# Optimization experiments

Hardware: AMD Instinct MI355X
Metric: run time of the kernel (lower is better)

Reference implementation:

```python
import jax, jax.numpy as jnp
import numpy as np

ACT = jax.nn.leaky_relu  # Decima uses leaky_relu activations


def _mlp(x, params):
    # Linear + act chain (activation applied after every layer, incl. last, as in the torch code)
    for W, b in params:
        x = ACT(x @ W + b)
    return x


def setup_inputs() -> dict:
    key = jax.random.key(0)
    N, E, D = 500_000, 4_000_000, 8  # nodes, edges per depth, max_depth
    ks = jax.random.split(key, 32)
    inp = {}
    inp["inputs"] = jax.random.normal(ks[0], (N, 5), dtype=jnp.float32)
    inp["adj_src"] = jax.random.randint(ks[1], (D, E), 0, N, dtype=jnp.int32)
    inp["adj_dst"] = jax.random.randint(ks[2], (D, E), 0, N, dtype=jnp.int32)
    inp["masks"] = (jax.random.uniform(ks[3], (D, N, 1)) > 0.5).astype(jnp.float32)
    # MLP stacks: prep 5->16->32->8, proc/agg 8->16->32->8 (xavier-ish init, zero bias)
    dims = {"prep": [(5, 16), (16, 32), (32, 8)],
            "proc": [(8, 16), (16, 32), (32, 8)],
            "agg": [(8, 16), (16, 32), (32, 8)]}
    i = 4
    for name, ds in dims.items():
        for j, (a, b) in enumerate(ds):
            scale = np.sqrt(6.0 / (a + b)).astype(np.float32)
            inp[f"{name}_W{j}"] = jax.random.uniform(ks[i], (a, b), jnp.float32, -scale, scale)
            inp[f"{name}_b{j}"] = jnp.zeros((b,), jnp.float32)
            i += 1
    return inp


def reference(inputs, adj_src, adj_dst, masks,
              prep_W0, prep_b0, prep_W1, prep_b1, prep_W2, prep_b2,
              proc_W0, proc_b0, proc_W1, proc_b1, proc_W2, proc_b2,
              agg_W0, agg_b0, agg_W1, agg_b1, agg_W2, agg_b2):
    prep = [(prep_W0, prep_b0), (prep_W1, prep_b1), (prep_W2, prep_b2)]
    proc = [(proc_W0, proc_b0), (proc_W1, proc_b1), (proc_W2, proc_b2)]
    agg = [(agg_W0, agg_b0), (agg_W1, agg_b1), (agg_W2, agg_b2)]
    N = inputs.shape[0]
    max_depth = adj_src.shape[0]

    x = _mlp(inputs, prep)  # [N, 8]
    for d in range(max_depth):  # small fixed loop over depths
        y = _mlp(x, proc)  # [N, 8]
        # sparse adj matmul (unit-valued adjacency): out[i] = sum_{j: (i,j) in adj} y[j]
        y = jax.ops.segment_sum(y[adj_src[d]], adj_dst[d], num_segments=N)
        y = _mlp(y, agg)
        x = x + y * masks[d]  # mask + residual
    return x
```

## Files before the change

### kernel.cpp

```cpp
#include <hip/hip_runtime.h>
#include <hip/hip_fp16.h>


typedef unsigned long long u64;
typedef unsigned int u32;

#define BKT_BITS 10
#define BKT_SIZE 1024
#define MAXNB    512
#define NBLK     256

template <int CH> struct Cfg;
template <> struct Cfg<4> { static const int CAPC = 6;  static const int SUBC = 24; };
template <> struct Cfg<2> { static const int CAPC = 14; static const int SUBC = 32; };
template <> struct Cfg<1> { static const int CAPC = 30; static const int SUBC = 64; };

__device__ __forceinline__ float lrelu(float v) { return fmaxf(v, 0.01f * v); }

template <int IN>
__device__ __forceinline__ void mlp3(const float* __restrict__ xin, float* __restrict__ yout,
    const float* __restrict__ sW0, const float* __restrict__ sb0,
    const float* __restrict__ sW1, const float* __restrict__ sb1,
    const float* __restrict__ sW2, const float* __restrict__ sb2)
{
    float h1[16];
#pragma unroll
    for (int o = 0; o < 16; ++o) {
        float s = sb0[o];
#pragma unroll
        for (int a = 0; a < IN; ++a) s = fmaf(xin[a], sW0[a * 16 + o], s);
        h1[o] = lrelu(s);
    }
    float h2[32];
#pragma unroll
    for (int o = 0; o < 32; ++o) {
        float s = sb1[o];
#pragma unroll
        for (int a = 0; a < 16; ++a) s = fmaf(h1[a], sW1[a * 32 + o], s);
        h2[o] = lrelu(s);
    }
#pragma unroll
    for (int o = 0; o < 8; ++o) {
        float s = sb2[o];
#pragma unroll
        for (int a = 0; a < 32; ++a) s = fmaf(h2[a], sW2[a * 8 + o], s);
        yout[o] = lrelu(s);
    }
}

__device__ __forceinline__ void ldw(float* d, const float* s, int n) {
    for (int t = threadIdx.x; t < n; t += 256) d[t] = s[t];
}

__device__ __forceinline__ uint4 pack_h8(const float* y) {
    __half2 p0 = __floats2half2_rn(y[0], y[1]);
    __half2 p1 = __floats2half2_rn(y[2], y[3]);
    __half2 p2 = __floats2half2_rn(y[4], y[5]);
    __half2 p3 = __floats2half2_rn(y[6], y[7]);
    uint4 v;
    v.x = *(u32*)&p0; v.y = *(u32*)&p1; v.z = *(u32*)&p2; v.w = *(u32*)&p3;
    return v;
}

__global__ __launch_bounds__(256) void prep_proc_kernel(
    const float* __restrict__ in, float* __restrict__ x, uint4* __restrict__ y,
    const float* pW0, const float* pb0, const float* pW1, const float* pb1,
    const float* pW2, const float* pb2,
    const float* cW0, const float* cb0, const float* cW1, const float* cb1,
    const float* cW2, const float* cb2, int N)
{
    __shared__ float P0[80],  Pb0[16], P1[512], Pb1[32], P2[256], Pb2[8];
    __shared__ float C0[128], Cb0[16], C1[512], Cb1[32], C2[256], Cb2[8];
    ldw(P0, pW0, 80);  ldw(Pb0, pb0, 16); ldw(P1, pW1, 512); ldw(Pb1, pb1, 32);
    ldw(P2, pW2, 256); ldw(Pb2, pb2, 8);
    ldw(C0, cW0, 128); ldw(Cb0, cb0, 16); ldw(C1, cW1, 512); ldw(Cb1, cb1, 32);
    ldw(C2, cW2, 256); ldw(Cb2, cb2, 8);
    __syncthreads();
    int i = blockIdx.x * 256 + threadIdx.x;
    if (i >= N) return;
    float xin[5];
#pragma unroll
    for (int k = 0; k < 5; ++k) xin[k] = in[(size_t)i * 5 + k];
    float xv[8];
    mlp3<5>(xin, xv, P0, Pb0, P1, Pb1, P2, Pb2);
    float4* xp = (float4*)(x + 8 * (size_t)i);
    xp[0] = make_float4(xv[0], xv[1], xv[2], xv[3]);
    xp[1] = make_float4(xv[4], xv[5], xv[6], xv[7]);
    float yv[8];
    mlp3<8>(xv, yv, C0, Cb0, C1, Cb1, C2, Cb2);
    y[i] = pack_h8(yv);
}

template <bool DO_PROC, int CHUNKS>
__global__ __launch_bounds__(256) void aggproc_kernel(
    const uint4* __restrict__ acc, float* __restrict__ x, const float* __restrict__ mask,
    uint4* __restrict__ y,
    const float* aW0, const float* ab0, const float* aW1, const float* ab1,
    const float* aW2, const float* ab2,
    const float* cW0, const float* cb0, const float* cW1, const float* cb1,
    const float* cW2, const float* cb2, int N)
{
    __shared__ float A0[128], Ab0[16], A1[512], Ab1[32], A2[256], Ab2[8];
    __shared__ float C0[128], Cb0[16], C1[512], Cb1[32], C2[256], Cb2[8];
    ldw(A0, aW0, 128); ldw(Ab0, ab0, 16); ldw(A1, aW1, 512); ldw(Ab1, ab1, 32);
    ldw(A2, aW2, 256); ldw(Ab2, ab2, 8);
    if (DO_PROC) {
        ldw(C0, cW0, 128); ldw(Cb0, cb0, 16); ldw(C1, cW1, 512); ldw(Cb1, cb1, 32);
        ldw(C2, cW2, 256); ldw(Cb2, cb2, 8);
    }
    __syncthreads();
    int i = blockIdx.x * 256 + threadIdx.x;
    if (i >= N) return;
    float ain[8] = {0.f, 0.f, 0.f, 0.f, 0.f, 0.f, 0.f, 0.f};
#pragma unroll
    for (int c = 0; c < CHUNKS; ++c) {
        uint4 v = acc[(size_t)c * N + i];
        float2 f0 = __half22float2(*(__half2*)&v.x);
        float2 f1 = __half22float2(*(__half2*)&v.y);
        float2 f2 = __half22float2(*(__half2*)&v.z);
        float2 f3 = __half22float2(*(__half2*)&v.w);
        ain[0] += f0.x; ain[1] += f0.y; ain[2] += f1.x; ain[3] += f1.y;
        ain[4] += f2.x; ain[5] += f2.y; ain[6] += f3.x; ain[7] += f3.y;
    }
    float ya[8];
    mlp3<8>(ain, ya, A0, Ab0, A1, Ab1, A2, Ab2);
    float m = mask[i];
    float4* xp = (float4*)(x + 8 * (size_t)i);
    float4 x0 = xp[0], x1 = xp[1];
    float xn[8] = {x0.x + ya[0] * m, x0.y + ya[1] * m, x0.z + ya[2] * m, x0.w + ya[3] * m,
                   x1.x + ya[4] * m, x1.y + ya[5] * m, x1.z + ya[6] * m, x1.w + ya[7] * m};
    xp[0] = make_float4(xn[0], xn[1], xn[2], xn[3]);
    xp[1] = make_float4(xn[4], xn[5], xn[6], xn[7]);
    if (DO_PROC) {
        float yv[8];
        mlp3<8>(xn, yv, C0, Cb0, C1, Cb1, C2, Cb2);
        y[i] = pack_h8(yv);
    }
}

__global__ __launch_bounds__(256) void mask_pack_kernel(
    const float* __restrict__ masks, u64* __restrict__ bitmaps, int N, int D, int BITW)
{
    int i = blockIdx.x * 256 + threadIdx.x;
    int lane = threadIdx.x & 63;
    for (int d = 0; d < D; ++d) {
        bool b = (i < N) ? (masks[(size_t)d * N + i] != 0.f) : false;
        u64 m = __ballot(b);
        if (lane == 0 && i < N) bitmaps[(size_t)d * BITW + (i >> 6)] = m;
    }
}

template <int CHUNKS>
__global__ __launch_bounds__(256) void place_kernel(
    const int* __restrict__ adj_src, const int* __restrict__ adj_dst,
    const u64* __restrict__ bitmaps,
    u32* __restrict__ ebuf_all,
    int* __restrict__ cnt_all,
    int E, int NB, int shift, int BITW)
{
    constexpr int CAPC = Cfg<CHUNKS>::CAPC;
    constexpr int SUBC = Cfg<CHUNKS>::SUBC;
    const int dep = blockIdx.y;
    const int* src = adj_src + (size_t)dep * E;
    const int* dst = adj_dst + (size_t)dep * E;
    const u64* bitmap = bitmaps + (size_t)dep * BITW;
    u32* ebuf = ebuf_all + (size_t)dep * ((size_t)NB * CHUNKS * NBLK * SUBC);
    int* cnt_g = cnt_all + (size_t)dep * ((size_t)NB * CHUNKS * NBLK);

    __shared__ int lcnt[MAXNB * CHUNKS];
    __shared__ u32 stage[MAXNB * CHUNKS * CAPC];
    const int cells = NB * CHUNKS;
    for (int t = threadIdx.x; t < cells; t += 256) lcnt[t] = 0;
    __syncthreads();

    const int blk = blockIdx.x;
    const int E4 = E >> 2;
    const int CH4 = (E4 + NBLK - 1) / NBLK;
    const int base4 = blk * CH4;
    const int lim4 = min(base4 + CH4, E4);
    const int4* src4 = (const int4*)src;
    const int4* dst4 = (const int4*)dst;

#define PLACE(dv, sv) { int _d = (dv); \
    if ((bitmap[_d >> 6] >> (_d & 63)) & 1ull) { \
        int _cell = (_d >> BKT_BITS) * CHUNKS + ((u32)(sv) >> shift); \
        int _slot = atomicAdd(&lcnt[_cell], 1); \
        u32 _w = ((u32)(sv) << BKT_BITS) | (u32)(_d & (BKT_SIZE - 1)); \
        if (_slot < CAPC) stage[_cell * CAPC + _slot] = _w; \
        else if (_slot < SUBC) ebuf[((size_t)_cell * NBLK + blk) * SUBC + _slot] = _w; \
    } }

    for (int i4 = base4 + threadIdx.x; i4 < lim4; i4 += 256) {
        int4 dv = dst4[i4];
        int4 sv = src4[i4];
        PLACE(dv.x, sv.x) PLACE(dv.y, sv.y) PLACE(dv.z, sv.z) PLACE(dv.w, sv.w)
    }
    if (blk == NBLK - 1)
        for (int e = (E4 << 2) + threadIdx.x; e < E; e += 256) { PLACE(dst[e], src[e]) }
#undef PLACE

    __syncthreads();
    constexpr int SLOTW = (CAPC <= 8) ? 8 : (CAPC <= 16) ? 16 : 32;
    constexpr int CPW = 64 / SLOTW;
    int wave = threadIdx.x >> 6, lane = threadIdx.x & 63;
    int cslot = lane % SLOTW, coff = lane / SLOTW;
    for (int c0 = wave * CPW; c0 < cells; c0 += 4 * CPW) {
        int cell = c0 + coff;
        if (cell < cells) {
            int n = lcnt[cell];
            int ns = min(n, CAPC);
            size_t gb = ((size_t)cell * NBLK + blk) * SUBC;
            if (cslot < ns) ebuf[gb + cslot] = stage[cell * CAPC + cslot];
            if (cslot == 0) cnt_g[cell * NBLK + blk] = min(n, SUBC);
        }
    }
}

__device__ __forceinline__ void accum4(__half2* __restrict__ sacc, u32 w, uint4 v)
{
    int dl = (int)(w & (BKT_SIZE - 1));
    __half2* a = sacc + dl * 5;
    unsafeAtomicAdd(a + 0, *(__half2*)&v.x);
    unsafeAtomicAdd(a + 1, *(__half2*)&v.y);
    unsafeAtomicAdd(a + 2, *(__half2*)&v.z);
    unsafeAtomicAdd(a + 3, *(__half2*)&v.w);
}

template <int CHUNKS>
__global__ __launch_bounds__(256) void reduce_kernel(
    const uint4* __restrict__ y, const u32* __restrict__ ebuf, const int* __restrict__ cnt_g,
    uint4* __restrict__ acc, int N, int NB)
{
    constexpr int SUBC = Cfg<CHUNKS>::SUBC;
    int i = blockIdx.x, bucket, chunk;
    if (CHUNKS == 4)      { bucket = (i >> 3) * 2 + (i & 1); chunk = (i >> 1) & 3; }
    else if (CHUNKS == 2) { bucket = (i >> 3) * 4 + (i & 3); chunk = (i >> 2) & 1; }
    else                  { bucket = i; chunk = 0; }
    if (bucket >= NB) return;

    __shared__ __half2 sacc[BKT_SIZE * 5];
    for (int t = threadIdx.x; t < BKT_SIZE * 5; t += 256) ((u32*)sacc)[t] = 0u;
    __syncthreads();

    int cell = bucket * CHUNKS + chunk;
    int sb = cell * NBLK + threadIdx.x;
    int n = cnt_g[sb];
    const u32* r = ebuf + (size_t)sb * SUBC;

    int k = 0;
    for (; k + 3 < n; k += 4) {
        u32 w0 = r[k], w1 = r[k + 1], w2 = r[k + 2], w3 = r[k + 3];
        uint4 v0 = y[w0 >> BKT_BITS];
        uint4 v1 = y[w1 >> BKT_BITS];
        uint4 v2 = y[w2 >> BKT_BITS];
        uint4 v3 = y[w3 >> BKT_BITS];
        accum4(sacc, w0, v0);
        accum4(sacc, w1, v1);
        accum4(sacc, w2, v2);
        accum4(sacc, w3, v3);
    }
    for (; k < n; ++k) {
        u32 w = r[k];
        uint4 v = y[w >> BKT_BITS];
        accum4(sacc, w, v);
    }

    __syncthreads();
    int node0 = bucket << BKT_BITS;
    uint4* accc = acc + (size_t)chunk * N;
    for (int t = threadIdx.x; t < BKT_SIZE; t += 256) {
        int idx = node0 + t;
        if (idx < N) {
            __half2* a = sacc + t * 5;
            uint4 o;
            o.x = *(u32*)(a + 0); o.y = *(u32*)(a + 1);
            o.z = *(u32*)(a + 2); o.w = *(u32*)(a + 3);
            accc[idx] = o;
        }
    }
}

__global__ __launch_bounds__(256) void scatter_kernel(
    const uint4* __restrict__ y, const int* __restrict__ src, const int* __restrict__ dst,
    const float* __restrict__ mask, __half2* __restrict__ acc, int E)
{
    int e = blockIdx.x * blockDim.x + threadIdx.x;
    if (e >= E) return;
    int d = dst[e];
    if (mask[d] == 0.f) return;
    int s = src[e];
    uint4 v = y[s];
    __half2* o = acc + 4 * (size_t)d;
    unsafeAtomicAdd(o + 0, *(__half2*)&v.x);
    unsafeAtomicAdd(o + 1, *(__half2*)&v.y);
    unsafeAtomicAdd(o + 2, *(__half2*)&v.z);
    unsafeAtomicAdd(o + 3, *(__half2*)&v.w);
}

template <int CH>
static void run_fast(hipStream_t stream, bool batch, int N, int E, int D, int NB, int shift,
                     int BITW, int nbN,
                     const int* adj_src, const int* adj_dst, const float* masks,
                     const u64* bitmaps, u32* ebuf, int* cnt_g,
                     uint4* y, uint4* acc, float* x,
                     const float* aW0, const float* ab0, const float* aW1, const float* ab1,
                     const float* aW2, const float* ab2,
                     const float* cW0, const float* cb0, const float* cW1, const float* cb1,
                     const float* cW2, const float* cb2)
{
    constexpr int SUBC = Cfg<CH>::SUBC;
    const size_t EB = (size_t)NB * CH * NBLK * SUBC;
    const size_t CN = (size_t)NB * CH * NBLK;
    const int rgrid = (CH == 4) ? ((NB + 1) / 2) * 8 : (CH == 2) ? ((NB + 3) / 4) * 8 : NB;

    if (batch)
        place_kernel<CH><<<dim3(NBLK, D), 256, 0, stream>>>(adj_src, adj_dst, bitmaps,
                                                            ebuf, cnt_g, E, NB, shift, BITW);

    for (int d = 0; d < D; ++d) {
        const float* mask_d = masks + (size_t)d * N;
        if (!batch)
            place_kernel<CH><<<dim3(NBLK, 1), 256, 0, stream>>>(
                adj_src + (size_t)d * E, adj_dst + (size_t)d * E, bitmaps + (size_t)d * BITW,
                ebuf, cnt_g, E, NB, shift, BITW);
        const u32* eb_d = ebuf + (batch ? (size_t)d * EB : 0);
        const int* cg_d = cnt_g + (batch ? (size_t)d * CN : 0);
        reduce_kernel<CH><<<rgrid, 256, 0, stream>>>(y, eb_d, cg_d, acc, N, NB);
        if (d < D - 1)
            aggproc_kernel<true, CH><<<nbN, 256, 0, stream>>>(acc, x, mask_d, y,
                aW0, ab0, aW1, ab1, aW2, ab2, cW0, cb0, cW1, cb1, cW2, cb2, N);
        else
            aggproc_kernel<false, CH><<<nbN, 256, 0, stream>>>(acc, x, mask_d, y,
                aW0, ab0, aW1, ab1, aW2, ab2, cW0, cb0, cW1, cb1, cW2, cb2, N);
    }
}

extern "C" void kernel_launch(void* const* d_in, const int* in_sizes, int n_in,
                              void* d_out, int out_size, void* d_ws, size_t ws_size,
                              hipStream_t stream)
{
    const float* inputs  = (const float*)d_in[0];
    const int*   adj_src = (const int*)d_in[1];
    const int*   adj_dst = (const int*)d_in[2];
    const float* masks   = (const float*)d_in[3];

    const float* pW0 = (const float*)d_in[4];  const float* pb0 = (const float*)d_in[5];
    const float* pW1 = (const float*)d_in[6];  const float* pb1 = (const float*)d_in[7];
    const float* pW2 = (const float*)d_in[8];  const float* pb2 = (const float*)d_in[9];
    const float* cW0 = (const float*)d_in[10]; const float* cb0 = (const float*)d_in[11];
    const float* cW1 = (const float*)d_in[12]; const float* cb1 = (const float*)d_in[13];
    const float* cW2 = (const float*)d_in[14]; const float* cb2 = (const float*)d_in[15];
    const float* aW0 = (const float*)d_in[16]; const float* ab0 = (const float*)d_in[17];
    const float* aW1 = (const float*)d_in[18]; const float* ab1 = (const float*)d_in[19];
    const float* aW2 = (const float*)d_in[20]; const float* ab2 = (const float*)d_in[21];

    const int N = in_sizes[0] / 5;
    const int D = in_sizes[3] / N;
    const int E = in_sizes[1] / D;
    const int NB = (N + BKT_SIZE - 1) >> BKT_BITS;
    const int BITW = (N + 63) >> 6;

    float* x = (float*)d_out;

    auto layout_bytes = [&](int ch, bool batch) -> size_t {
        int subc = (ch == 4) ? 24 : (ch == 2) ? 32 : 64;
        int nd = batch ? D : 1;
        size_t s = 0;
        auto al = [&](size_t b) { s = (s + b + 255) & ~(size_t)255; };
        al((size_t)N * 16);
        al((size_t)ch * N * 16);
        al((size_t)D * BITW * 8);
        al((size_t)nd * NB * ch * NBLK * subc * 4);
        al((size_t)nd * NB * ch * NBLK * 4);
        return s;
    };
    int CHsel = 0; bool batch = false;
    if (NB <= MAXNB) {
        struct Opt { int ch; bool b; };
        const Opt opts[6] = {{4,true},{2,true},{1,true},{4,false},{2,false},{1,false}};
        for (int k = 0; k < 6; ++k)
            if (layout_bytes(opts[k].ch, opts[k].b) <= ws_size) { CHsel = opts[k].ch; batch = opts[k].b; break; }
    }
    bool fast = CHsel > 0;
    int subc = (CHsel == 4) ? 24 : (CHsel == 2) ? 32 : 64;
    int nd = batch ? D : 1;

    char* w = (char*)d_ws;
    size_t off = 0;
    auto take = [&](size_t bytes) { char* p = w + off; off = (off + bytes + 255) & ~(size_t)255; return p; };
    uint4* y   = (uint4*)take((size_t)N * 16);
    uint4* acc = (uint4*)take((size_t)(fast ? CHsel : 1) * N * 16);
    u64* bitmaps = (u64*)take((size_t)D * BITW * 8);
    u32* ebuf  = fast ? (u32*)take((size_t)nd * NB * CHsel * NBLK * subc * 4) : nullptr;
    int* cnt_g = fast ? (int*)take((size_t)nd * NB * CHsel * NBLK * 4) : nullptr;

    int shift = 0;
    if (fast) { while ((u32)(N - 1) >> shift >= (u32)CHsel) shift++; }

    const int BLK = 256;
    const int nbN = (N + BLK - 1) / BLK;
    const int nbE = (E + BLK - 1) / BLK;

    if (fast)
        mask_pack_kernel<<<nbN, BLK, 0, stream>>>(masks, bitmaps, N, D, BITW);

    prep_proc_kernel<<<nbN, BLK, 0, stream>>>(inputs, x, y,
                                              pW0, pb0, pW1, pb1, pW2, pb2,
                                              cW0, cb0, cW1, cb1, cW2, cb2, N);

    if (fast) {
        if (CHsel == 4)
            run_fast<4>(stream, batch, N, E, D, NB, shift, BITW, nbN, adj_src, adj_dst, masks,
                        bitmaps, ebuf, cnt_g, y, acc, x,
                        aW0, ab0, aW1, ab1, aW2, ab2, cW0, cb0, cW1, cb1, cW2, cb2);
        else if (CHsel == 2)
            run_fast<2>(stream, batch, N, E, D, NB, shift, BITW, nbN, adj_src, adj_dst, masks,
                        bitmaps, ebuf, cnt_g, y, acc, x,
                        aW0, ab0, aW1, ab1, aW2, ab2, cW0, cb0, cW1, cb1, cW2, cb2);
        else
            run_fast<1>(stream, batch, N, E, D, NB, shift, BITW, nbN, adj_src, adj_dst, masks,
                        bitmaps, ebuf, cnt_g, y, acc, x,
                        aW0, ab0, aW1, ab1, aW2, ab2, cW0, cb0, cW1, cb1, cW2, cb2);
    } else {
        for (int d = 0; d < D; ++d) {
            const float* mask_d = masks + (size_t)d * N;
            const int* src_d = adj_src + (size_t)d * E;
            const int* dst_d = adj_dst + (size_t)d * E;
            bool last = (d == D - 1);
            hipMemsetAsync(acc, 0, (size_t)N * 16, stream);
            scatter_kernel<<<nbE, BLK, 0, stream>>>(y, src_d, dst_d, mask_d, (__half2*)acc, E);
            if (!last)
                aggproc_kernel<true, 1><<<nbN, BLK, 0, stream>>>(acc, x, mask_d, y,
                    aW0, ab0, aW1, ab1, aW2, ab2, cW0, cb0, cW1, cb1, cW2, cb2, N);
            else
                aggproc_kernel<false, 1><<<nbN, BLK, 0, stream>>>(acc, x, mask_d, y,
                    aW0, ab0, aW1, ab1, aW2, ab2, cW0, cb0, cW1, cb1, cW2, cb2, N);
        }
    }
}
```

Before: 1.345 ms.

## Merge two buckets per reduce block for CH=4 and shrink LDS staging capacity

```diff
diff --git a/kernel.cpp b/kernel.cpp
--- a/kernel.cpp
+++ b/kernel.cpp
@@ -11,7 +11,7 @@
 #define NBLK     256
 
 template <int CH> struct Cfg;
-template <> struct Cfg<4> { static const int CAPC = 6;  static const int SUBC = 24; };
+template <> struct Cfg<4> { static const int CAPC = 4;  static const int SUBC = 24; };
 template <> struct Cfg<2> { static const int CAPC = 14; static const int SUBC = 32; };
 template <> struct Cfg<1> { static const int CAPC = 30; static const int SUBC = 64; };
 
@@ -200,7 +200,7 @@
 #undef PLACE
 
     __syncthreads();
-    constexpr int SLOTW = (CAPC <= 8) ? 8 : (CAPC <= 16) ? 16 : 32;
+    constexpr int SLOTW = (CAPC <= 4) ? 4 : (CAPC <= 8) ? 8 : (CAPC <= 16) ? 16 : 32;
     constexpr int CPW = 64 / SLOTW;
     int wave = threadIdx.x >> 6, lane = threadIdx.x & 63;
     int cslot = lane % SLOTW, coff = lane / SLOTW;
@@ -232,46 +232,94 @@
     uint4* __restrict__ acc, int N, int NB)
 {
     constexpr int SUBC = Cfg<CHUNKS>::SUBC;
-    int i = blockIdx.x, bucket, chunk;
-    if (CHUNKS == 4)      { bucket = (i >> 3) * 2 + (i & 1); chunk = (i >> 1) & 3; }
-    else if (CHUNKS == 2) { bucket = (i >> 3) * 4 + (i & 3); chunk = (i >> 2) & 1; }
-    else                  { bucket = i; chunk = 0; }
-    if (bucket >= NB) return;
-
-    __shared__ __half2 sacc[BKT_SIZE * 5];
-    for (int t = threadIdx.x; t < BKT_SIZE * 5; t += 256) ((u32*)sacc)[t] = 0u;
-    __syncthreads();
-
-    int cell = bucket * CHUNKS + chunk;
-    int sb = cell * NBLK + threadIdx.x;
-    int n = cnt_g[sb];
-    const u32* r = ebuf + (size_t)sb * SUBC;
-
-    int k = 0;
-    for (; k + 3 < n; k += 4) {
-        u32 w0 = r[k], w1 = r[k + 1], w2 = r[k + 2], w3 = r[k + 3];
-        uint4 v0 = y[w0 >> BKT_BITS];
-        uint4 v1 = y[w1 >> BKT_BITS];
-        uint4 v2 = y[w2 >> BKT_BITS];
-        uint4 v3 = y[w3 >> BKT_BITS];
-        accum4(sacc, w0, v0);
-        accum4(sacc, w1, v1);
-        accum4(sacc, w2, v2);
-        accum4(sacc, w3, v3);
-    }
-    for (; k < n; ++k) {
-        u32 w = r[k];
-        uint4 v = y[w >> BKT_BITS];
-        accum4(sacc, w, v);
-    }
-
-    __syncthreads();
-    int node0 = bucket << BKT_BITS;
+    constexpr int NODES = (CHUNKS == 4) ? 2 * BKT_SIZE : BKT_SIZE;
+    __shared__ __half2 sacc[NODES * 5];
+
+    int b0, chunk;
+    if (CHUNKS == 4) {
+        int i = blockIdx.x, q = i >> 3, r = i & 7;
+        chunk = r >> 1;
+        int pair = q * 2 + (r & 1);
+        b0 = pair * 2;
+        if (b0 >= NB) return;
+    } else if (CHUNKS == 2) {
+        int i = blockIdx.x;
+        b0 = (i >> 3) * 4 + (i & 3); chunk = (i >> 2) & 1;
+        if (b0 >= NB) return;
+    } else {
+        b0 = blockIdx.x; chunk = 0;
+        if (b0 >= NB) return;
+    }
+
+    for (int t = threadIdx.x; t < NODES * 5; t += 256) ((u32*)sacc)[t] = 0u;
+    __syncthreads();
+
+    int t = threadIdx.x;
+    if (CHUNKS == 4) {
+        int cell0 = b0 * CHUNKS + chunk;
+        int sb0 = cell0 * NBLK + t;
+        int n0 = cnt_g[sb0];
+        const u32* r0 = ebuf + (size_t)sb0 * SUBC;
+        bool has1 = (b0 + 1 < NB);
+        int sb1 = (cell0 + CHUNKS) * NBLK + t;
+        int n1 = has1 ? cnt_g[sb1] : 0;
+        const u32* r1 = ebuf + (size_t)sb1 * SUBC;
+        int total = n0 + n1;
+
+#define LD(kk, w, o) { int _k = (kk); const u32* _p; \
+    if (_k < n0) { _p = r0 + _k; o = 0; } else { _p = r1 + (_k - n0); o = 5 * BKT_SIZE; } \
+    w = *_p; }
+        int k = 0;
+        for (; k + 3 < total; k += 4) {
+            u32 w0, w1, w2, w3; int o0, o1, o2, o3;
+            LD(k, w0, o0) LD(k + 1, w1, o1) LD(k + 2, w2, o2) LD(k + 3, w3, o3)
+            uint4 v0 = y[w0 >> BKT_BITS];
+            uint4 v1 = y[w1 >> BKT_BITS];
+            uint4 v2 = y[w2 >> BKT_BITS];
+            uint4 v3 = y[w3 >> BKT_BITS];
+            accum4(sacc + o0, w0, v0);
+            accum4(sacc + o1, w1, v1);
+            accum4(sacc + o2, w2, v2);
+            accum4(sacc + o3, w3, v3);
+        }
+        for (; k < total; ++k) {
+            u32 w; int o;
+            LD(k, w, o)
+            uint4 v = y[w >> BKT_BITS];
+            accum4(sacc + o, w, v);
+        }
+#undef LD
+    } else {
+        int cell = b0 * CHUNKS + chunk;
+        int sb = cell * NBLK + t;
+        int n = cnt_g[sb];
+        const u32* r = ebuf + (size_t)sb * SUBC;
+        int k = 0;
+        for (; k + 3 < n; k += 4) {
+            u32 w0 = r[k], w1 = r[k + 1], w2 = r[k + 2], w3 = r[k + 3];
+            uint4 v0 = y[w0 >> BKT_BITS];
+            uint4 v1 = y[w1 >> BKT_BITS];
+            uint4 v2 = y[w2 >> BKT_BITS];
+            uint4 v3 = y[w3 >> BKT_BITS];
+            accum4(sacc, w0, v0);
+            accum4(sacc, w1, v1);
+            accum4(sacc, w2, v2);
+            accum4(sacc, w3, v3);
+        }
+        for (; k < n; ++k) {
+            u32 w = r[k];
+            uint4 v = y[w >> BKT_BITS];
+            accum4(sacc, w, v);
+        }
+    }
+
+    __syncthreads();
+    int node0 = b0 << BKT_BITS;
     uint4* accc = acc + (size_t)chunk * N;
-    for (int t = threadIdx.x; t < BKT_SIZE; t += 256) {
-        int idx = node0 + t;
+    for (int t2 = threadIdx.x; t2 < NODES; t2 += 256) {
+        int idx = node0 + t2;
         if (idx < N) {
-            __half2* a = sacc + t * 5;
+            __half2* a = sacc + t2 * 5;
             uint4 o;
             o.x = *(u32*)(a + 0); o.y = *(u32*)(a + 1);
             o.z = *(u32*)(a + 2); o.w = *(u32*)(a + 3);
@@ -311,7 +359,8 @@
     constexpr int SUBC = Cfg<CH>::SUBC;
     const size_t EB = (size_t)NB * CH * NBLK * SUBC;
     const size_t CN = (size_t)NB * CH * NBLK;
-    const int rgrid = (CH == 4) ? ((NB + 1) / 2) * 8 : (CH == 2) ? ((NB + 3) / 4) * 8 : NB;
+    const int rgrid = (CH == 4) ? ((((NB + 1) / 2) + 1) / 2) * 8
+                    : (CH == 2) ? ((NB + 3) / 4) * 8 : NB;
 
     if (batch)
         place_kernel<CH><<<dim3(NBLK, D), 256, 0, stream>>>(adj_src, adj_dst, bitmaps,
```

New measurement: 1.378 ms. +2.4%, slower.
